# Kernel optimization log

Measured on AMD Instinct MI355X. Metric: run time of the kernel, lower is better.

Reference implementation:

```python
import jax, jax.numpy as jnp
import numpy as np

N_ENT = 50000
N_REL = 16
N_EDGE = 1000000
D = 64


def setup_inputs() -> dict:
    key = jax.random.key(0)
    ks = jax.random.split(key, 20)
    inp = {
        'ent_embed': jax.random.normal(ks[0], (N_ENT, D), jnp.float32) * 0.1,
        'rel_embed': jax.random.normal(ks[1], (N_REL, D), jnp.float32) * 0.1,
        'W_R': jax.random.normal(ks[2], (N_REL, D, D), jnp.float32) * 0.1,
        'W1_0': jax.random.normal(ks[3], (64, 64), jnp.float32) * 0.1,
        'b1_0': jax.random.normal(ks[4], (64,), jnp.float32) * 0.1,
        'W2_0': jax.random.normal(ks[5], (64, 64), jnp.float32) * 0.1,
        'b2_0': jax.random.normal(ks[6], (64,), jnp.float32) * 0.1,
        'W1_1': jax.random.normal(ks[7], (64, 32), jnp.float32) * 0.1,
        'b1_1': jax.random.normal(ks[8], (32,), jnp.float32) * 0.1,
        'W2_1': jax.random.normal(ks[9], (64, 32), jnp.float32) * 0.1,
        'b2_1': jax.random.normal(ks[10], (32,), jnp.float32) * 0.1,
        'W1_2': jax.random.normal(ks[11], (32, 16), jnp.float32) * 0.1,
        'b1_2': jax.random.normal(ks[12], (16,), jnp.float32) * 0.1,
        'W2_2': jax.random.normal(ks[13], (32, 16), jnp.float32) * 0.1,
        'b2_2': jax.random.normal(ks[14], (16,), jnp.float32) * 0.1,
        'src': jax.random.randint(ks[15], (N_EDGE,), 0, N_ENT, jnp.int32),
        'dst': jax.random.randint(ks[16], (N_EDGE,), 0, N_ENT, jnp.int32),
        'etype': jax.random.randint(ks[17], (N_EDGE,), 0, N_REL, jnp.int32),
    }
    return inp


def _l2_normalize(x, eps=1e-12):
    # matches torch F.normalize(p=2, dim=1)
    n = jnp.sqrt(jnp.sum(x * x, axis=1, keepdims=True))
    return x / jnp.maximum(n, eps)


def _kgat_forward(ent_embed, rel_embed, W_R, layer_params, src, dst, etype):
    N = ent_embed.shape[0]
    # --- compute_attention: per-relation TransR projection of all entities ---
    # equivalent to per-edge ent[src] @ W_R[type] without materializing [E, D, D]
    proj = jnp.einsum('nd,rde->rne', ent_embed, W_R)          # [R, N, D]
    r_mul_t = proj[etype, src]                                # [E, D] (tail = src)
    r_mul_h = proj[etype, dst]                                # [E, D] (head = dst)
    att = jnp.sum(r_mul_t * jnp.tanh(r_mul_h + rel_embed[etype]), axis=-1)  # [E]
    # edge softmax grouped by destination node
    m = jax.ops.segment_max(att, dst, num_segments=N)         # [N]
    e = jnp.exp(att - m[dst])
    s = jax.ops.segment_sum(e, dst, num_segments=N)           # [N]
    a = e / s[dst]                                            # [E]

    # --- cf_embedding: bi-interaction aggregator layers ---
    h = ent_embed
    all_embed = [h]
    for (W1, b1, W2, b2) in layer_params:
        msg = a[:, None] * h[src]                             # [E, d_in]
        N_h = jax.ops.segment_sum(msg, dst, num_segments=N)   # [N, d_in]
        out = (jax.nn.leaky_relu((h + N_h) @ W1 + b1, 0.01)
               + jax.nn.leaky_relu((h * N_h) @ W2 + b2, 0.01))
        h = out
        all_embed.append(_l2_normalize(out))
    return jnp.concatenate(all_embed, axis=1)                 # [N, 64+64+32+16=176]


def reference(ent_embed, rel_embed, W_R,
              W1_0, b1_0, W2_0, b2_0,
              W1_1, b1_1, W2_1, b2_1,
              W1_2, b1_2, W2_2, b2_2,
              src, dst, etype):
    layer_params = [(W1_0, b1_0, W2_0, b2_0),
                    (W1_1, b1_1, W2_1, b2_1),
                    (W1_2, b1_2, W2_2, b2_2)]
    return _kgat_forward(ent_embed, rel_embed, W_R, layer_params, src, dst, etype)
```

## Files before the change

kernel.cpp:

```cpp
#include <hip/hip_runtime.h>
#include <hip/hip_bf16.h>
#include <cmath>

#define N_ENT  50000
#define N_RELS 16
#define N_EDGE 1000000
#define DIM    64
#define OUT_STRIDE 176

typedef float f32x4 __attribute__((ext_vector_type(4)));
typedef short s16x8 __attribute__((ext_vector_type(8)));

__device__ inline void bf16x8_unpack(uint4 u, float* f) {
    f[0] = __uint_as_float((u.x & 0xffffu) << 16);
    f[1] = __uint_as_float(u.x & 0xffff0000u);
    f[2] = __uint_as_float((u.y & 0xffffu) << 16);
    f[3] = __uint_as_float(u.y & 0xffff0000u);
    f[4] = __uint_as_float((u.z & 0xffffu) << 16);
    f[5] = __uint_as_float(u.z & 0xffff0000u);
    f[6] = __uint_as_float((u.w & 0xffffu) << 16);
    f[7] = __uint_as_float(u.w & 0xffff0000u);
}

__device__ inline ushort f2bf(float x) {
    __hip_bfloat16 b = __float2bfloat16(x);
    return *(ushort*)&b;
}

__global__ __launch_bounds__(256) void prep_hist_kernel(
        const float* __restrict__ ent,
        ushort* __restrict__ ent_bf,
        ushort* __restrict__ p0, ushort* __restrict__ p1,
        float* __restrict__ out,
        const int* __restrict__ dst, int* __restrict__ counts) {
    int i = blockIdx.x * blockDim.x + threadIdx.x;
    if (i < N_ENT * DIM) {
        float v = ent[i];
        ushort b = f2bf(v);
        int n = i >> 6, c = i & 63;
        ent_bf[i] = b;
        if (c < 32) p0[n * 32 + c] = b;
        else        p1[n * 32 + (c - 32)] = b;
        out[(size_t)n * OUT_STRIDE + c] = v;
    }
    if (i < N_EDGE) atomicAdd(&counts[dst[i]], 1);
}

__global__ __launch_bounds__(256) void scan1_kernel(
        const int* __restrict__ counts, int* __restrict__ excl,
        int* __restrict__ bsum, int n) {
    __shared__ int sh[256];
    int t = threadIdx.x;
    int i = blockIdx.x * 256 + t;
    int c = (i < n) ? counts[i] : 0;
    sh[t] = c;
    __syncthreads();
    for (int off = 1; off < 256; off <<= 1) {
        int v = (t >= off) ? sh[t - off] : 0;
        __syncthreads();
        sh[t] += v;
        __syncthreads();
    }
    if (i < n) excl[i] = sh[t] - c;
    if (t == 255) bsum[blockIdx.x] = sh[255];
}

__global__ __launch_bounds__(256) void scan2_kernel(
        const int* __restrict__ bsum, int* __restrict__ boff,
        int* __restrict__ row_ptr, int nb, int n) {
    __shared__ int sh[256];
    int t = threadIdx.x;
    int v = (t < nb) ? bsum[t] : 0;
    sh[t] = v;
    __syncthreads();
    for (int off = 1; off < 256; off <<= 1) {
        int x = (t >= off) ? sh[t - off] : 0;
        __syncthreads();
        sh[t] += x;
        __syncthreads();
    }
    if (t < nb) boff[t] = sh[t] - v;
    if (t == nb - 1) row_ptr[n] = sh[t];
}

__global__ __launch_bounds__(256) void scan3_kernel(
        const int* __restrict__ excl, const int* __restrict__ boff,
        int* __restrict__ row_ptr, int n) {
    int i = blockIdx.x * blockDim.x + threadIdx.x;
    if (i < n) row_ptr[i] = excl[i] + boff[i >> 8];
}

__global__ __launch_bounds__(256) void gz_mfma_kernel(
        const ushort* __restrict__ ent_bf,
        const float*  __restrict__ W_R,
        const float*  __restrict__ rel,
        __hip_bfloat16* __restrict__ Z) {
    __shared__ float lds[4][16 * 68 + 16];
    int lane = threadIdx.x & 63;
    int wv   = threadIdx.x >> 6;
    int m    = lane & 15;
    int q    = lane >> 4;
    int r    = blockIdx.y;
    int wid  = blockIdx.x * 4 + wv;
    int nw   = gridDim.x * 4;

    const float* Wr = W_R + (size_t)r * DIM * DIM;
    s16x8 b1[4][2], b2[4][2];
#pragma unroll
    for (int c = 0; c < 4; ++c)
#pragma unroll
        for (int ch = 0; ch < 2; ++ch)
#pragma unroll
            for (int j = 0; j < 8; ++j) {
                b1[c][ch][j] = (short)f2bf(Wr[(ch * 32 + q * 8 + j) * DIM + c * 16 + m]);
                b2[c][ch][j] = (short)f2bf(Wr[(c * 16 + m) * DIM + ch * 32 + q * 8 + j]);
            }
    float relv[4];
#pragma unroll
    for (int c = 0; c < 4; ++c) relv[c] = rel[r * DIM + c * 16 + m];

    float* myLds = lds[wv];
    const int ntiles = N_ENT / 16;

    for (int t = wid; t < ntiles; t += nw) {
        int row0 = t * 16;
        const s16x8* arow = (const s16x8*)(ent_bf + (size_t)(row0 + m) * DIM);
        s16x8 a0 = arow[q];
        s16x8 a1 = arow[4 + q];
        f32x4 acc[4];
#pragma unroll
        for (int c = 0; c < 4; ++c) acc[c] = (f32x4){0.f, 0.f, 0.f, 0.f};
#pragma unroll
        for (int c = 0; c < 4; ++c) {
            acc[c] = __builtin_amdgcn_mfma_f32_16x16x32_bf16(a0, b1[c][0], acc[c], 0, 0, 0);
            acc[c] = __builtin_amdgcn_mfma_f32_16x16x32_bf16(a1, b1[c][1], acc[c], 0, 0, 0);
        }
#pragma unroll
        for (int c = 0; c < 4; ++c)
#pragma unroll
            for (int i = 0; i < 4; ++i) {
                float x = acc[c][i] + relv[c];
                float g = 1.f - 2.f / (__expf(2.f * x) + 1.f);
                myLds[(q * 4 + i) * 68 + c * 16 + m] = g;
            }
        s16x8 a2[2];
#pragma unroll
        for (int ch = 0; ch < 2; ++ch)
#pragma unroll
            for (int j = 0; j < 8; ++j)
                a2[ch][j] = (short)f2bf(myLds[m * 68 + ch * 32 + q * 8 + j]);

        f32x4 zacc[4];
#pragma unroll
        for (int c = 0; c < 4; ++c) zacc[c] = (f32x4){0.f, 0.f, 0.f, 0.f};
#pragma unroll
        for (int c = 0; c < 4; ++c) {
            zacc[c] = __builtin_amdgcn_mfma_f32_16x16x32_bf16(a2[0], b2[c][0], zacc[c], 0, 0, 0);
            zacc[c] = __builtin_amdgcn_mfma_f32_16x16x32_bf16(a2[1], b2[c][1], zacc[c], 0, 0, 0);
        }
        __hip_bfloat16* zrow = Z + ((size_t)r * N_ENT + row0) * DIM;
#pragma unroll
        for (int c = 0; c < 4; ++c)
#pragma unroll
            for (int i = 0; i < 4; ++i)
                zrow[(q * 4 + i) * DIM + c * 16 + m] = __float2bfloat16(zacc[c][i]);
    }
}

__global__ __launch_bounds__(256) void att_dot_kernel(
        const ushort* __restrict__ ent_bf,
        const __hip_bfloat16* __restrict__ Z,
        const int* __restrict__ src,
        const int* __restrict__ dst,
        const int* __restrict__ etype,
        const int* __restrict__ row_ptr,
        int* __restrict__ cursor,
        uint2* __restrict__ es_csr,
        int n_edge) {
    int tid  = blockIdx.x * blockDim.x + threadIdx.x;
    int lane = threadIdx.x & 63;
    int sub  = lane >> 3;
    int q    = lane & 7;
    int e    = (tid >> 6) * 8 + sub;
    if (e >= n_edge) return;

    int s = src[e];
    int d = dst[e];
    int r = etype[e];

    uint4 uz = *(const uint4*)(Z + ((size_t)r * N_ENT + d) * DIM + q * 8);
    uint4 ue = *(const uint4*)(ent_bf + (size_t)s * DIM + q * 8);

    float zv[8], ev[8];
    bf16x8_unpack(uz, zv);
    bf16x8_unpack(ue, ev);

    float prod = 0.f;
#pragma unroll
    for (int j = 0; j < 8; ++j) prod = fmaf(ev[j], zv[j], prod);
    prod += __shfl_xor(prod, 1, 64);
    prod += __shfl_xor(prod, 2, 64);
    prod += __shfl_xor(prod, 4, 64);

    if (q == 0) {
        int pos = row_ptr[d] + atomicAdd(&cursor[d], 1);
        es_csr[pos] = make_uint2(__float_as_uint(prod), (unsigned)s);
    }
}

__global__ __launch_bounds__(256) void softmax_kernel(
        const int* __restrict__ row_ptr, uint2* __restrict__ es_csr, int n_node) {
    int wid  = (blockIdx.x * blockDim.x + threadIdx.x) >> 6;
    int lane = threadIdx.x & 63;
    if (wid >= n_node) return;
    int start = row_ptr[wid], end = row_ptr[wid + 1];

    float m = -INFINITY;
    for (int i = start + lane; i < end; i += 64)
        m = fmaxf(m, __uint_as_float(es_csr[i].x));
#pragma unroll
    for (int off = 32; off > 0; off >>= 1)
        m = fmaxf(m, __shfl_xor(m, off, 64));

    float ssum = 0.f;
    for (int i = start + lane; i < end; i += 64) {
        float e = expf(__uint_as_float(es_csr[i].x) - m);
        es_csr[i].x = __float_as_uint(e);
        ssum += e;
    }
#pragma unroll
    for (int off = 32; off > 0; off >>= 1)
        ssum += __shfl_xor(ssum, off, 64);

    if (end > start) {
        float inv = 1.0f / ssum;
        for (int i = start + lane; i < end; i += 64) {
            float a = __uint_as_float(es_csr[i].x) * inv;
            es_csr[i].x = __float_as_uint(a);
        }
    }
}

__global__ __launch_bounds__(256) void agg_kernel(
        const ushort* __restrict__ plane,
        const uint2* __restrict__ es_csr,
        const int* __restrict__ row_ptr,
        float* __restrict__ N_h, int stride, int off, int n_node) {
    int wid  = (blockIdx.x * blockDim.x + threadIdx.x) >> 6;
    int lane = threadIdx.x & 63;
    if (wid >= n_node) return;
    int q   = lane & 3;
    int sub = lane >> 2;

    int start = row_ptr[wid], end = row_ptr[wid + 1];
    float acc[8];
#pragma unroll
    for (int j = 0; j < 8; ++j) acc[j] = 0.f;

    for (int p = start + sub; p < end; p += 16) {
        uint2 es = es_csr[p];
        float av = __uint_as_float(es.x);
        int   si = (int)es.y;
        uint4 u  = *(const uint4*)(plane + (size_t)si * 32 + q * 8);
        float g[8];
        bf16x8_unpack(u, g);
#pragma unroll
        for (int j = 0; j < 8; ++j) acc[j] = fmaf(av, g[j], acc[j]);
    }
#pragma unroll
    for (int mask = 4; mask < 64; mask <<= 1)
#pragma unroll
        for (int j = 0; j < 8; ++j)
            acc[j] += __shfl_xor(acc[j], mask, 64);

    if (sub == 0) {
        float* dstp = N_h + (size_t)wid * stride + off + q * 8;
        *(float4*)(dstp)     = (float4){acc[0], acc[1], acc[2], acc[3]};
        *(float4*)(dstp + 4) = (float4){acc[4], acc[5], acc[6], acc[7]};
    }
}

template <int D_IN, int D_OUT>
__global__ __launch_bounds__(256) void mlp_mfma_kernel(
        const ushort* __restrict__ h_p0,
        const ushort* __restrict__ h_p1,
        const float* __restrict__ N_h,
        const float* __restrict__ W1, const float* __restrict__ b1,
        const float* __restrict__ W2, const float* __restrict__ b2,
        ushort* __restrict__ ho_p0,
        ushort* __restrict__ ho_p1,
        float* __restrict__ out_buf, int out_col) {
    constexpr int CH = D_IN / 32;
    constexpr int CT = D_OUT / 16;

    int lane = threadIdx.x & 63;
    int m    = lane & 15;
    int q    = lane >> 4;
    int wid  = blockIdx.x * (blockDim.x >> 6) + (threadIdx.x >> 6);
    int nw   = gridDim.x * (blockDim.x >> 6);

    s16x8 bu[CT][CH], bv[CT][CH];
#pragma unroll
    for (int c = 0; c < CT; ++c)
#pragma unroll
        for (int ch = 0; ch < CH; ++ch)
#pragma unroll
            for (int j = 0; j < 8; ++j) {
                int k = ch * 32 + q * 8 + j;
                bu[c][ch][j] = (short)f2bf(W1[k * D_OUT + c * 16 + m]);
                bv[c][ch][j] = (short)f2bf(W2[k * D_OUT + c * 16 + m]);
            }

    const int ntiles = N_ENT / 16;
    for (int t = wid; t < ntiles; t += nw) {
        int row0 = t * 16;
        s16x8 au[CH], av[CH];
#pragma unroll
        for (int ch = 0; ch < CH; ++ch) {
            const ushort* hp = (ch == 0) ? h_p0 : h_p1;
            uint4 hu = *(const uint4*)(hp + (size_t)(row0 + m) * 32 + q * 8);
            float hv8[8];
            bf16x8_unpack(hu, hv8);
            const float4* np = (const float4*)(N_h + (size_t)(row0 + m) * D_IN + ch * 32 + q * 8);
            float4 na = np[0], nb = np[1];
            float nv[8] = {na.x, na.y, na.z, na.w, nb.x, nb.y, nb.z, nb.w};
#pragma unroll
            for (int j = 0; j < 8; ++j) {
                au[ch][j] = (short)f2bf(hv8[j] + nv[j]);
                av[ch][j] = (short)f2bf(hv8[j] * nv[j]);
            }
        }

        f32x4 accu[CT], accv[CT];
#pragma unroll
        for (int c = 0; c < CT; ++c) {
            accu[c] = (f32x4){0.f, 0.f, 0.f, 0.f};
            accv[c] = (f32x4){0.f, 0.f, 0.f, 0.f};
        }
#pragma unroll
        for (int c = 0; c < CT; ++c)
#pragma unroll
            for (int ch = 0; ch < CH; ++ch) {
                accu[c] = __builtin_amdgcn_mfma_f32_16x16x32_bf16(au[ch], bu[c][ch], accu[c], 0, 0, 0);
                accv[c] = __builtin_amdgcn_mfma_f32_16x16x32_bf16(av[ch], bv[c][ch], accv[c], 0, 0, 0);
            }

        float res[CT][4];
        float sq[4] = {0.f, 0.f, 0.f, 0.f};
#pragma unroll
        for (int c = 0; c < CT; ++c) {
            float bb1 = b1[c * 16 + m];
            float bb2 = b2[c * 16 + m];
#pragma unroll
            for (int i = 0; i < 4; ++i) {
                float o1 = accu[c][i] + bb1;
                float o2 = accv[c][i] + bb2;
                float r1 = (o1 >= 0.f) ? o1 : 0.01f * o1;
                float r2 = (o2 >= 0.f) ? o2 : 0.01f * o2;
                float rr = r1 + r2;
                res[c][i] = rr;
                sq[i] = fmaf(rr, rr, sq[i]);
            }
        }
#pragma unroll
        for (int mask = 1; mask < 16; mask <<= 1)
#pragma unroll
            for (int i = 0; i < 4; ++i)
                sq[i] += __shfl_xor(sq[i], mask, 64);

#pragma unroll
        for (int i = 0; i < 4; ++i) {
            int row = row0 + q * 4 + i;
            float inv = 1.f / fmaxf(sqrtf(sq[i]), 1e-12f);
#pragma unroll
            for (int c = 0; c < CT; ++c) {
                int col = c * 16 + m;
                out_buf[(size_t)row * OUT_STRIDE + out_col + col] = res[c][i] * inv;
                if (ho_p0) {
                    ushort hb = f2bf(res[c][i]);
                    if (col < 32) ho_p0[(size_t)row * 32 + col] = hb;
                    else          ho_p1[(size_t)row * 32 + (col - 32)] = hb;
                }
            }
        }
    }
}

extern "C" void kernel_launch(void* const* d_in, const int* in_sizes, int n_in,
                              void* d_out, int out_size, void* d_ws, size_t ws_size,
                              hipStream_t stream) {
    const float* ent  = (const float*)d_in[0];
    const float* rel  = (const float*)d_in[1];
    const float* W_R  = (const float*)d_in[2];
    const float* W1_0 = (const float*)d_in[3];
    const float* b1_0 = (const float*)d_in[4];
    const float* W2_0 = (const float*)d_in[5];
    const float* b2_0 = (const float*)d_in[6];
    const float* W1_1 = (const float*)d_in[7];
    const float* b1_1 = (const float*)d_in[8];
    const float* W2_1 = (const float*)d_in[9];
    const float* b2_1 = (const float*)d_in[10];
    const float* W1_2 = (const float*)d_in[11];
    const float* b1_2 = (const float*)d_in[12];
    const float* W2_2 = (const float*)d_in[13];
    const float* b2_2 = (const float*)d_in[14];
    const int*   src   = (const int*)d_in[15];
    const int*   dst   = (const int*)d_in[16];
    const int*   etype = (const int*)d_in[17];
    float* out = (float*)d_out;

    char* w = (char*)d_ws;
    uint2*  es_csr  = (uint2*)w;  w += (size_t)N_EDGE * 8;
    int*    counts  = (int*)w;    w += (size_t)(N_ENT + 64) * 4;
    int*    row_ptr = (int*)w;    w += (size_t)(N_ENT + 64) * 4;
    int*    cursor  = (int*)w;    w += (size_t)(N_ENT + 64) * 4;
    int*    excl    = (int*)w;    w += (size_t)(N_ENT + 64) * 4;
    int*    bsum    = (int*)w;    w += 256 * 4;
    int*    boff    = (int*)w;    w += 256 * 4;
    ushort* ent_bf  = (ushort*)w; w += (size_t)N_ENT * 64 * 2;
    ushort* ent_p0  = (ushort*)w; w += (size_t)N_ENT * 32 * 2;
    ushort* ent_p1  = (ushort*)w; w += (size_t)N_ENT * 32 * 2;
    ushort* h1_p0   = (ushort*)w; w += (size_t)N_ENT * 32 * 2;
    ushort* h1_p1   = (ushort*)w; w += (size_t)N_ENT * 32 * 2;
    ushort* h2      = (ushort*)w; w += (size_t)N_ENT * 32 * 2;
    float*  N_h     = (float*)w;  w += (size_t)N_ENT * 64 * 4;
    __hip_bfloat16* Z = (__hip_bfloat16*)w;
    (void)ws_size;

    hipMemsetAsync(counts, 0, (size_t)N_ENT * 4, stream);
    hipMemsetAsync(cursor, 0, (size_t)N_ENT * 4, stream);

    const int nb = (N_ENT + 255) / 256;

    prep_hist_kernel<<<(N_ENT * DIM + 255) / 256, 256, 0, stream>>>(
        ent, ent_bf, ent_p0, ent_p1, out, dst, counts);
    scan1_kernel<<<nb, 256, 0, stream>>>(counts, excl, bsum, N_ENT);
    scan2_kernel<<<1, 256, 0, stream>>>(bsum, boff, row_ptr, nb, N_ENT);
    scan3_kernel<<<nb, 256, 0, stream>>>(excl, boff, row_ptr, N_ENT);

    gz_mfma_kernel<<<dim3(64, N_RELS), 256, 0, stream>>>(ent_bf, W_R, rel, Z);
    att_dot_kernel<<<((N_EDGE + 7) / 8 * 64 + 255) / 256, 256, 0, stream>>>(
        ent_bf, Z, src, dst, etype, row_ptr, cursor, es_csr, N_EDGE);

    softmax_kernel<<<(N_ENT + 3) / 4, 256, 0, stream>>>(row_ptr, es_csr, N_ENT);

    const int aggGrid = (N_ENT + 3) / 4;
    const int mlpGrid = 782;

    agg_kernel<<<aggGrid, 256, 0, stream>>>(ent_p0, es_csr, row_ptr, N_h, 64, 0,  N_ENT);
    agg_kernel<<<aggGrid, 256, 0, stream>>>(ent_p1, es_csr, row_ptr, N_h, 64, 32, N_ENT);
    mlp_mfma_kernel<64, 64><<<mlpGrid, 256, 0, stream>>>(
        ent_p0, ent_p1, N_h, W1_0, b1_0, W2_0, b2_0, h1_p0, h1_p1, out, 64);

    agg_kernel<<<aggGrid, 256, 0, stream>>>(h1_p0, es_csr, row_ptr, N_h, 64, 0,  N_ENT);
    agg_kernel<<<aggGrid, 256, 0, stream>>>(h1_p1, es_csr, row_ptr, N_h, 64, 32, N_ENT);
    mlp_mfma_kernel<64, 32><<<mlpGrid, 256, 0, stream>>>(
        h1_p0, h1_p1, N_h, W1_1, b1_1, W2_1, b2_1, h2, nullptr, out, 128);

    agg_kernel<<<aggGrid, 256, 0, stream>>>(h2, es_csr, row_ptr, N_h, 32, 0, N_ENT);
    mlp_mfma_kernel<32, 16><<<mlpGrid, 256, 0, stream>>>(
        h2, nullptr, N_h, W1_2, b1_2, W2_2, b2_2, nullptr, nullptr, out, 160);
}
```

Before: 423.3 us.

## Precompute CSR edge slots in histogram and defer softmax normalization to aggregation

The histogram pass now keeps the return value of its atomic increment as each edge's offset within its destination row. A merged scan kernel then computes every edge's final CSR position and packs src, dst, etype and position into one 64-bit word. This removes the second atomic cursor pass and the separate src/dst/etype/row_ptr loads from the attention kernel, which now handles two edges per lane group. Softmax no longer rewrites the normalized weights; it stores one inverse sum per node, and the aggregation kernels scale their result by it. The packing relies on entity ids fitting in 16 bits, and the offset and packed-edge scratch arrays reuse the Z and N_h buffers before those are written.

```diff
diff --git a/kernel.cpp b/kernel.cpp
--- a/kernel.cpp
+++ b/kernel.cpp
@@ -32,7 +32,8 @@
         ushort* __restrict__ ent_bf,
         ushort* __restrict__ p0, ushort* __restrict__ p1,
         float* __restrict__ out,
-        const int* __restrict__ dst, int* __restrict__ counts) {
+        const int* __restrict__ dst, int* __restrict__ counts,
+        int* __restrict__ off) {
     int i = blockIdx.x * blockDim.x + threadIdx.x;
     if (i < N_ENT * DIM) {
         float v = ent[i];
@@ -43,7 +44,7 @@
         else        p1[n * 32 + (c - 32)] = b;
         out[(size_t)n * OUT_STRIDE + c] = v;
     }
-    if (i < N_EDGE) atomicAdd(&counts[dst[i]], 1);
+    if (i < N_EDGE) off[i] = atomicAdd(&counts[dst[i]], 1);
 }
 
 __global__ __launch_bounds__(256) void scan1_kernel(
@@ -83,11 +84,24 @@
     if (t == nb - 1) row_ptr[n] = sh[t];
 }
 
-__global__ __launch_bounds__(256) void scan3_kernel(
+__global__ __launch_bounds__(256) void scan3_pos_kernel(
         const int* __restrict__ excl, const int* __restrict__ boff,
-        int* __restrict__ row_ptr, int n) {
+        int* __restrict__ row_ptr,
+        const int* __restrict__ src, const int* __restrict__ dst,
+        const int* __restrict__ etype, const int* __restrict__ off,
+        unsigned long long* __restrict__ einfo) {
     int i = blockIdx.x * blockDim.x + threadIdx.x;
-    if (i < n) row_ptr[i] = excl[i] + boff[i >> 8];
+    if (i < N_ENT) row_ptr[i] = excl[i] + boff[i >> 8];
+    if (i < N_EDGE) {
+        int d = dst[i];
+        int pos = excl[d] + boff[d >> 8] + off[i];
+        unsigned long long info =
+              (unsigned long long)(unsigned)src[i]
+            | ((unsigned long long)(unsigned)d << 16)
+            | ((unsigned long long)(unsigned)etype[i] << 32)
+            | ((unsigned long long)(unsigned)pos << 36);
+        einfo[i] = info;
+    }
 }
 
 __global__ __launch_bounds__(256) void gz_mfma_kernel(
@@ -170,46 +184,63 @@
 __global__ __launch_bounds__(256) void att_dot_kernel(
         const ushort* __restrict__ ent_bf,
         const __hip_bfloat16* __restrict__ Z,
-        const int* __restrict__ src,
-        const int* __restrict__ dst,
-        const int* __restrict__ etype,
-        const int* __restrict__ row_ptr,
-        int* __restrict__ cursor,
+        const unsigned long long* __restrict__ einfo,
         uint2* __restrict__ es_csr,
         int n_edge) {
     int tid  = blockIdx.x * blockDim.x + threadIdx.x;
     int lane = threadIdx.x & 63;
     int sub  = lane >> 3;
     int q    = lane & 7;
-    int e    = (tid >> 6) * 8 + sub;
-    if (e >= n_edge) return;
-
-    int s = src[e];
-    int d = dst[e];
-    int r = etype[e];
-
-    uint4 uz = *(const uint4*)(Z + ((size_t)r * N_ENT + d) * DIM + q * 8);
-    uint4 ue = *(const uint4*)(ent_bf + (size_t)s * DIM + q * 8);
-
-    float zv[8], ev[8];
-    bf16x8_unpack(uz, zv);
-    bf16x8_unpack(ue, ev);
-
-    float prod = 0.f;
-#pragma unroll
-    for (int j = 0; j < 8; ++j) prod = fmaf(ev[j], zv[j], prod);
-    prod += __shfl_xor(prod, 1, 64);
-    prod += __shfl_xor(prod, 2, 64);
-    prod += __shfl_xor(prod, 4, 64);
+    int base = (tid >> 6) * 16;
+    int e0 = base + sub;
+    int e1 = base + 8 + sub;
+    if (e0 >= n_edge) return;
+    bool v1 = (e1 < n_edge);
+    unsigned long long i0 = einfo[e0];
+    unsigned long long i1 = v1 ? einfo[e1] : i0;
+
+    int s0 = (int)(i0 & 0xffffu);
+    int d0 = (int)((i0 >> 16) & 0xffffu);
+    int r0 = (int)((i0 >> 32) & 0xfu);
+    int p0 = (int)(i0 >> 36);
+    int s1 = (int)(i1 & 0xffffu);
+    int d1 = (int)((i1 >> 16) & 0xffffu);
+    int r1 = (int)((i1 >> 32) & 0xfu);
+    int p1 = (int)(i1 >> 36);
+
+    uint4 uz0 = *(const uint4*)(Z + ((size_t)r0 * N_ENT + d0) * DIM + q * 8);
+    uint4 ue0 = *(const uint4*)(ent_bf + (size_t)s0 * DIM + q * 8);
+    uint4 uz1 = *(const uint4*)(Z + ((size_t)r1 * N_ENT + d1) * DIM + q * 8);
+    uint4 ue1 = *(const uint4*)(ent_bf + (size_t)s1 * DIM + q * 8);
+
+    float z0[8], w0[8], z1[8], w1[8];
+    bf16x8_unpack(uz0, z0);
+    bf16x8_unpack(ue0, w0);
+    bf16x8_unpack(uz1, z1);
+    bf16x8_unpack(ue1, w1);
+
+    float pr0 = 0.f, pr1 = 0.f;
+#pragma unroll
+    for (int j = 0; j < 8; ++j) {
+        pr0 = fmaf(w0[j], z0[j], pr0);
+        pr1 = fmaf(w1[j], z1[j], pr1);
+    }
+    pr0 += __shfl_xor(pr0, 1, 64);
+    pr1 += __shfl_xor(pr1, 1, 64);
+    pr0 += __shfl_xor(pr0, 2, 64);
+    pr1 += __shfl_xor(pr1, 2, 64);
+    pr0 += __shfl_xor(pr0, 4, 64);
+    pr1 += __shfl_xor(pr1, 4, 64);
 
     if (q == 0) {
-        int pos = row_ptr[d] + atomicAdd(&cursor[d], 1);
-        es_csr[pos] = make_uint2(__float_as_uint(prod), (unsigned)s);
+        es_csr[p0] = make_uint2(__float_as_uint(pr0), (unsigned)s0);
+        if (v1) es_csr[p1] = make_uint2(__float_as_uint(pr1), (unsigned)s1);
     }
 }
 
 __global__ __launch_bounds__(256) void softmax_kernel(
-        const int* __restrict__ row_ptr, uint2* __restrict__ es_csr, int n_node) {
+        const int* __restrict__ row_ptr, uint2* __restrict__ es_csr,
+        float* __restrict__ inv_sum, int n_node) {
     int wid  = (blockIdx.x * blockDim.x + threadIdx.x) >> 6;
     int lane = threadIdx.x & 63;
     if (wid >= n_node) return;
@@ -232,19 +263,15 @@
     for (int off = 32; off > 0; off >>= 1)
         ssum += __shfl_xor(ssum, off, 64);
 
-    if (end > start) {
-        float inv = 1.0f / ssum;
-        for (int i = start + lane; i < end; i += 64) {
-            float a = __uint_as_float(es_csr[i].x) * inv;
-            es_csr[i].x = __float_as_uint(a);
-        }
-    }
+    if (lane == 0)
+        inv_sum[wid] = (end > start) ? (1.0f / ssum) : 0.f;
 }
 
 __global__ __launch_bounds__(256) void agg_kernel(
         const ushort* __restrict__ plane,
         const uint2* __restrict__ es_csr,
         const int* __restrict__ row_ptr,
+        const float* __restrict__ inv_sum,
         float* __restrict__ N_h, int stride, int off, int n_node) {
     int wid  = (blockIdx.x * blockDim.x + threadIdx.x) >> 6;
     int lane = threadIdx.x & 63;
@@ -253,6 +280,7 @@
     int sub = lane >> 2;
 
     int start = row_ptr[wid], end = row_ptr[wid + 1];
+    float inv = inv_sum[wid];
     float acc[8];
 #pragma unroll
     for (int j = 0; j < 8; ++j) acc[j] = 0.f;
@@ -275,8 +303,8 @@
 
     if (sub == 0) {
         float* dstp = N_h + (size_t)wid * stride + off + q * 8;
-        *(float4*)(dstp)     = (float4){acc[0], acc[1], acc[2], acc[3]};
-        *(float4*)(dstp + 4) = (float4){acc[4], acc[5], acc[6], acc[7]};
+        *(float4*)(dstp)     = (float4){acc[0] * inv, acc[1] * inv, acc[2] * inv, acc[3] * inv};
+        *(float4*)(dstp + 4) = (float4){acc[4] * inv, acc[5] * inv, acc[6] * inv, acc[7] * inv};
     }
 }
 
@@ -413,7 +441,7 @@
     uint2*  es_csr  = (uint2*)w;  w += (size_t)N_EDGE * 8;
     int*    counts  = (int*)w;    w += (size_t)(N_ENT + 64) * 4;
     int*    row_ptr = (int*)w;    w += (size_t)(N_ENT + 64) * 4;
-    int*    cursor  = (int*)w;    w += (size_t)(N_ENT + 64) * 4;
+    float*  inv_sum = (float*)w;  w += (size_t)(N_ENT + 64) * 4;
     int*    excl    = (int*)w;    w += (size_t)(N_ENT + 64) * 4;
     int*    bsum    = (int*)w;    w += 256 * 4;
     int*    boff    = (int*)w;    w += 256 * 4;
@@ -427,37 +455,40 @@
     __hip_bfloat16* Z = (__hip_bfloat16*)w;
     (void)ws_size;
 
+    int* off = (int*)Z;
+    unsigned long long* einfo = (unsigned long long*)N_h;
+
     hipMemsetAsync(counts, 0, (size_t)N_ENT * 4, stream);
-    hipMemsetAsync(cursor, 0, (size_t)N_ENT * 4, stream);
 
     const int nb = (N_ENT + 255) / 256;
 
     prep_hist_kernel<<<(N_ENT * DIM + 255) / 256, 256, 0, stream>>>(
-        ent, ent_bf, ent_p0, ent_p1, out, dst, counts);
+        ent, ent_bf, ent_p0, ent_p1, out, dst, counts, off);
     scan1_kernel<<<nb, 256, 0, stream>>>(counts, excl, bsum, N_ENT);
     scan2_kernel<<<1, 256, 0, stream>>>(bsum, boff, row_ptr, nb, N_ENT);
-    scan3_kernel<<<nb, 256, 0, stream>>>(excl, boff, row_ptr, N_ENT);
+    scan3_pos_kernel<<<(N_EDGE + 255) / 256, 256, 0, stream>>>(
+        excl, boff, row_ptr, src, dst, etype, off, einfo);
 
     gz_mfma_kernel<<<dim3(64, N_RELS), 256, 0, stream>>>(ent_bf, W_R, rel, Z);
-    att_dot_kernel<<<((N_EDGE + 7) / 8 * 64 + 255) / 256, 256, 0, stream>>>(
-        ent_bf, Z, src, dst, etype, row_ptr, cursor, es_csr, N_EDGE);
-
-    softmax_kernel<<<(N_ENT + 3) / 4, 256, 0, stream>>>(row_ptr, es_csr, N_ENT);
+    att_dot_kernel<<<(N_EDGE / 16 * 64 + 255) / 256, 256, 0, stream>>>(
+        ent_bf, Z, einfo, es_csr, N_EDGE);
+
+    softmax_kernel<<<(N_ENT + 3) / 4, 256, 0, stream>>>(row_ptr, es_csr, inv_sum, N_ENT);
 
     const int aggGrid = (N_ENT + 3) / 4;
     const int mlpGrid = 782;
 
-    agg_kernel<<<aggGrid, 256, 0, stream>>>(ent_p0, es_csr, row_ptr, N_h, 64, 0,  N_ENT);
-    agg_kernel<<<aggGrid, 256, 0, stream>>>(ent_p1, es_csr, row_ptr, N_h, 64, 32, N_ENT);
+    agg_kernel<<<aggGrid, 256, 0, stream>>>(ent_p0, es_csr, row_ptr, inv_sum, N_h, 64, 0,  N_ENT);
+    agg_kernel<<<aggGrid, 256, 0, stream>>>(ent_p1, es_csr, row_ptr, inv_sum, N_h, 64, 32, N_ENT);
     mlp_mfma_kernel<64, 64><<<mlpGrid, 256, 0, stream>>>(
         ent_p0, ent_p1, N_h, W1_0, b1_0, W2_0, b2_0, h1_p0, h1_p1, out, 64);
 
-    agg_kernel<<<aggGrid, 256, 0, stream>>>(h1_p0, es_csr, row_ptr, N_h, 64, 0,  N_ENT);
-    agg_kernel<<<aggGrid, 256, 0, stream>>>(h1_p1, es_csr, row_ptr, N_h, 64, 32, N_ENT);
+    agg_kernel<<<aggGrid, 256, 0, stream>>>(h1_p0, es_csr, row_ptr, inv_sum, N_h, 64, 0,  N_ENT);
+    agg_kernel<<<aggGrid, 256, 0, stream>>>(h1_p1, es_csr, row_ptr, inv_sum, N_h, 64, 32, N_ENT);
     mlp_mfma_kernel<64, 32><<<mlpGrid, 256, 0, stream>>>(
         h1_p0, h1_p1, N_h, W1_1, b1_1, W2_1, b2_1, h2, nullptr, out, 128);
 
-    agg_kernel<<<aggGrid, 256, 0, stream>>>(h2, es_csr, row_ptr, N_h, 32, 0, N_ENT);
+    agg_kernel<<<aggGrid, 256, 0, stream>>>(h2, es_csr, row_ptr, inv_sum, N_h, 32, 0, N_ENT);
     mlp_mfma_kernel<32, 16><<<mlpGrid, 256, 0, stream>>>(
         h2, nullptr, N_h, W1_2, b1_2, W2_2, b2_2, nullptr, nullptr, out, 160);
 }
```

New measurement: 412.9 us. 1.03x faster.
